# Performance work log

Measured on AMD Instinct MI355X. Metric: run time of the kernel, lower is better.

The kernel has to match this reference:

```python
import jax, jax.numpy as jnp
import numpy as np

TOP_K = 2

def setup_inputs() -> dict:
    key = jax.random.key(0)
    k1, k2 = jax.random.split(key)
    N, D, E = 16384, 2048, 64
    x = jax.random.normal(k1, (N, D), dtype=jnp.float32)
    W = jax.random.normal(k2, (D, E), dtype=jnp.float32) * (1.0 / np.sqrt(D))
    b = jnp.zeros((E,), dtype=jnp.float32)
    return {"x": x, "W": W, "b": b}

def reference(x, W, b):
    # gate linear: [N, D] @ [D, E] + [E]
    logits = jnp.einsum('nd,de->ne', x, W) + b
    gates = jax.nn.softmax(logits, axis=-1)
    topk_vals, topk_idx = jax.lax.top_k(gates, TOP_K)  # [N, k]
    N = gates.shape[0]
    rows = jnp.arange(N)[:, None]  # [N, 1] broadcast over k
    dispatch_mask = jnp.zeros_like(gates).at[rows, topk_idx].set(topk_vals)
    return dispatch_mask, topk_idx
```

## Files before the change

kernel.cpp:

```cpp
#include <hip/hip_runtime.h>
#include <math.h>

#define NROWS 16384
#define DDIM  2048
#define EEXP  64
#define RB    32
#define NST   8
#define CHSTRIDE 24576

typedef short        bf16x8 __attribute__((ext_vector_type(8)));
typedef float        f32x16 __attribute__((ext_vector_type(16)));
typedef float        f32x4  __attribute__((ext_vector_type(4)));
typedef unsigned int u32x4  __attribute__((ext_vector_type(4)));

union V4 { u32x4 u; bf16x8 s; };

static __device__ __forceinline__ void split3x2(float f0, float f1,
                                                unsigned int &p0, unsigned int &p1,
                                                unsigned int &p2) {
    unsigned int a0 = __float_as_uint(f0), b0 = __float_as_uint(f1);
    unsigned int ah = a0 & 0xffff0000u,   bh = b0 & 0xffff0000u;
    float fa1 = f0 - __uint_as_float(ah);
    float fb1 = f1 - __uint_as_float(bh);
    unsigned int a1 = __float_as_uint(fa1), b1 = __float_as_uint(fb1);
    unsigned int am = a1 & 0xffff0000u,     bm = b1 & 0xffff0000u;
    float fa2 = fa1 - __uint_as_float(am);
    float fb2 = fb1 - __uint_as_float(bm);
    p0 = (a0 >> 16) | bh;
    p1 = (a1 >> 16) | bm;
    p2 = (__float_as_uint(fa2) >> 16) | (__float_as_uint(fb2) & 0xffff0000u);
}

static __device__ __forceinline__ void cvt8(f32x4 u, f32x4 v, V4 &q0, V4 &q1, V4 &q2) {
    unsigned int a, b, c;
    split3x2(u[0], u[1], a, b, c); q0.u[0] = a; q1.u[0] = b; q2.u[0] = c;
    split3x2(u[2], u[3], a, b, c); q0.u[1] = a; q1.u[1] = b; q2.u[1] = c;
    split3x2(v[0], v[1], a, b, c); q0.u[2] = a; q1.u[2] = b; q2.u[2] = c;
    split3x2(v[2], v[3], a, b, c); q0.u[3] = a; q1.u[3] = b; q2.u[3] = c;
}

#define MM(ACC, A, B) ACC = __builtin_amdgcn_mfma_f32_32x32x16_bf16((A), (B), ACC, 0, 0, 0)

__global__ __launch_bounds__(256)
void wsplit_kernel(const float* __restrict__ W, unsigned char* __restrict__ ws) {
    const int t  = blockIdx.x * 256 + threadIdx.x;
    const int e  = t & 63;
    const int ko = t >> 6;
    const int k0 = ko * 8;
    f32x4 u, v;
#pragma unroll
    for (int j = 0; j < 4; ++j) u[j] = W[(size_t)(k0 + j) * EEXP + e];
#pragma unroll
    for (int j = 0; j < 4; ++j) v[j] = W[(size_t)(k0 + 4 + j) * EEXP + e];
    V4 q0, q1, q2;
    cvt8(u, v, q0, q1, q2);
    const int c  = k0 >> 6;
    const int kg = (k0 >> 4) & 3;
    const int h  = (k0 >> 3) & 1;
    const int et = e >> 5;
    const int ln = h * 32 + (e & 31);
    unsigned char* d = ws + (size_t)(((((c * 4 + kg) * 2 + et) * 64) + ln) * 48);
    *(u32x4*)(d +  0) = q0.u;
    *(u32x4*)(d + 16) = q1.u;
    *(u32x4*)(d + 32) = q2.u;
}

__global__ __launch_bounds__(512, 2)
void router_kernel(const float* __restrict__ x,
                   const unsigned char* __restrict__ wsplit,
                   const float* __restrict__ bias_v,
                   float* __restrict__ mask_out,
                   float* __restrict__ idx_out) {
    __shared__ __align__(16) float smem[16384];

    const int tid  = threadIdx.x;
    const int lane = tid & 63;
    const int w    = __builtin_amdgcn_readfirstlane(tid >> 6);
    const int kg   = w & 3;
    const int et   = w >> 2;
    const int l31  = lane & 31;
    const int h    = lane >> 5;

    const int bid  = blockIdx.x;
    const int bswz = (bid & 7) * ((int)gridDim.x >> 3) + (bid >> 3);
    const int row0 = bswz * RB;

    const int srow = 4 * w;

    const unsigned char* wp = wsplit + (size_t)(((kg * 2 + et) * 64 + lane) * 48);

    f32x16 accA, accB;
#pragma unroll
    for (int i = 0; i < 16; ++i) { accA[i] = 0.f; accB[i] = 0.f; }

    {
        f32x4 X0, X1, X2, X3;
        X0 = *(const f32x4*)(x + (size_t)(row0 + srow + 0) * DDIM + lane * 4);
        X1 = *(const f32x4*)(x + (size_t)(row0 + srow + 1) * DDIM + lane * 4);
        X2 = *(const f32x4*)(x + (size_t)(row0 + srow + 2) * DDIM + lane * 4);
        X3 = *(const f32x4*)(x + (size_t)(row0 + srow + 3) * DDIM + lane * 4);
#define XWR(I, V, B)                                                          \
        *(f32x4*)(smem + (B) * 8192 + (srow + I) * 256 +                      \
                  ((lane ^ ((srow + I) & 7)) << 2)) = V;
        XWR(0, X0, 0) XWR(1, X1, 0) XWR(2, X2, 0) XWR(3, X3, 0)
    }
    __syncthreads();

#pragma unroll 1
    for (int s = 0; s < NST; ++s) {
        const int  buf  = s & 1;
        const bool more = (s + 1) < NST;

        f32x4 X0, X1, X2, X3;
        if (more) {
            const float* xs = x + (size_t)(s + 1) * 256 + lane * 4;
            X0 = *(const f32x4*)(xs + (size_t)(row0 + srow + 0) * DDIM);
            X1 = *(const f32x4*)(xs + (size_t)(row0 + srow + 1) * DDIM);
            X2 = *(const f32x4*)(xs + (size_t)(row0 + srow + 2) * DDIM);
            X3 = *(const f32x4*)(xs + (size_t)(row0 + srow + 3) * DDIM);
        }

        const float* xb = smem + buf * 8192 + l31 * 256;
        const int xr = l31 & 7;
#pragma unroll
        for (int cc = 0; cc < 4; ++cc) {
            const int k0 = cc * 64 + kg * 16 + h * 8;
            const int bb = k0 >> 2;
            f32x4 lo = *(const f32x4*)(xb + (((bb    ) ^ xr) << 2));
            f32x4 hi = *(const f32x4*)(xb + (((bb + 1) ^ xr) << 2));
            const unsigned char* q = wp + (size_t)(s * 4 + cc) * CHSTRIDE;
            V4 b0, b1, b2;
            b0.u = *(const u32x4*)(q);
            b1.u = *(const u32x4*)(q + 16);
            b2.u = *(const u32x4*)(q + 32);
            V4 a0, a1, a2;
            cvt8(lo, hi, a0, a1, a2);
            MM(accA, a0.s, b0.s); MM(accB, a0.s, b1.s); MM(accA, a1.s, b0.s);
            MM(accB, a0.s, b2.s); MM(accA, a1.s, b1.s); MM(accB, a2.s, b0.s);
        }

        if (more) {
            const int nb = buf ^ 1;
            XWR(0, X0, nb) XWR(1, X1, nb) XWR(2, X2, nb) XWR(3, X3, nb)
        }
        __syncthreads();
    }

    float* ep = smem;
#pragma unroll
    for (int r = 0; r < 16; ++r) {
        const int rowl = (r & 3) + 8 * (r >> 2) + 4 * h;
        ep[kg * 2048 + rowl * 64 + et * 32 + l31] = accA[r] + accB[r];
    }
    __syncthreads();

    const float bias = bias_v[lane];
#pragma unroll
    for (int rr = 0; rr < 4; ++rr) {
        const int rl  = w * 4 + rr;
        const int row = row0 + rl;
        float logit = bias + ep[rl * 64 + lane]
                           + ep[2048 + rl * 64 + lane]
                           + ep[4096 + rl * 64 + lane]
                           + ep[6144 + rl * 64 + lane];

        float m = logit;
#pragma unroll
        for (int off = 32; off >= 1; off >>= 1) m = fmaxf(m, __shfl_xor(m, off));
        float ex = __expf(logit - m);
        float s = ex;
#pragma unroll
        for (int off = 32; off >= 1; off >>= 1) s += __shfl_xor(s, off);
        float gate = ex / s;

        float v1 = logit; int i1 = lane;
#pragma unroll
        for (int off = 32; off >= 1; off >>= 1) {
            float ov = __shfl_xor(v1, off);
            int   oi = __shfl_xor(i1, off);
            if (ov > v1 || (ov == v1 && oi < i1)) { v1 = ov; i1 = oi; }
        }
        float v2 = (lane == i1) ? -INFINITY : logit; int i2 = lane;
#pragma unroll
        for (int off = 32; off >= 1; off >>= 1) {
            float ov = __shfl_xor(v2, off);
            int   oi = __shfl_xor(i2, off);
            if (ov > v2 || (ov == v2 && oi < i2)) { v2 = ov; i2 = oi; }
        }

        float outv = (lane == i1 || lane == i2) ? gate : 0.0f;
        mask_out[(size_t)row * EEXP + lane] = outv;
        if (lane == 0) {
            idx_out[row * 2 + 0] = (float)i1;
            idx_out[row * 2 + 1] = (float)i2;
        }
    }
}

extern "C" void kernel_launch(void* const* d_in, const int* in_sizes, int n_in,
                              void* d_out, int out_size, void* d_ws, size_t ws_size,
                              hipStream_t stream) {
    const float* x = (const float*)d_in[0];
    const float* W = (const float*)d_in[1];
    const float* b = (const float*)d_in[2];
    float* mask_out = (float*)d_out;
    float* idx_out  = mask_out + (size_t)NROWS * EEXP;
    unsigned char* ws = (unsigned char*)d_ws;

    wsplit_kernel<<<dim3(64), dim3(256), 0, stream>>>(W, ws);
    router_kernel<<<dim3(NROWS / RB), dim3(512), 0, stream>>>(x, ws, b, mask_out, idx_out);
}
```

Measured before the change: 212.3 us.

## Double rows per block to reuse W fragments and stagger K-stage order

Each block now handles 64 rows instead of 32. Every wave keeps two sets of accumulators, so each W split fragment loaded from global memory feeds twice as many MFMAs. Blocks also start the K loop at different stages (s0 = block index mod 8) to spread W reads across memory channels. In exchange, LDS doubles to 128KB per block, accumulator and register pressure grow, and the grid is halved to 256 blocks, which may cut occupancy and parallelism on the 256-CU device.

```diff
diff --git a/kernel.cpp b/kernel.cpp
--- a/kernel.cpp
+++ b/kernel.cpp
@@ -4,7 +4,7 @@
 #define NROWS 16384
 #define DDIM  2048
 #define EEXP  64
-#define RB    32
+#define RB    64
 #define NST   8
 #define CHSTRIDE 24576
 
@@ -71,7 +71,7 @@
                    const float* __restrict__ bias_v,
                    float* __restrict__ mask_out,
                    float* __restrict__ idx_out) {
-    __shared__ __align__(16) float smem[16384];
+    __shared__ __align__(16) float smem[32768];
 
     const int tid  = threadIdx.x;
     const int lane = tid & 63;
@@ -84,64 +84,84 @@
     const int bid  = blockIdx.x;
     const int bswz = (bid & 7) * ((int)gridDim.x >> 3) + (bid >> 3);
     const int row0 = bswz * RB;
-
-    const int srow = 4 * w;
+    const int s0   = bswz & 7;
+
+    const int srow = 8 * w;
 
     const unsigned char* wp = wsplit + (size_t)(((kg * 2 + et) * 64 + lane) * 48);
 
-    f32x16 accA, accB;
-#pragma unroll
-    for (int i = 0; i < 16; ++i) { accA[i] = 0.f; accB[i] = 0.f; }
+    f32x16 accA, accB, accC, accD;
+#pragma unroll
+    for (int i = 0; i < 16; ++i) { accA[i] = 0.f; accB[i] = 0.f; accC[i] = 0.f; accD[i] = 0.f; }
+
+#define XWR(I, V, B, SR_ROW_BASE)                                             \
+    *(f32x4*)(smem + (B) * 16384 + (SR_ROW_BASE + I) * 256 +                  \
+              ((lane ^ ((SR_ROW_BASE + I) & 7)) << 2)) = V;
 
     {
-        f32x4 X0, X1, X2, X3;
-        X0 = *(const f32x4*)(x + (size_t)(row0 + srow + 0) * DDIM + lane * 4);
-        X1 = *(const f32x4*)(x + (size_t)(row0 + srow + 1) * DDIM + lane * 4);
-        X2 = *(const f32x4*)(x + (size_t)(row0 + srow + 2) * DDIM + lane * 4);
-        X3 = *(const f32x4*)(x + (size_t)(row0 + srow + 3) * DDIM + lane * 4);
-#define XWR(I, V, B)                                                          \
-        *(f32x4*)(smem + (B) * 8192 + (srow + I) * 256 +                      \
-                  ((lane ^ ((srow + I) & 7)) << 2)) = V;
-        XWR(0, X0, 0) XWR(1, X1, 0) XWR(2, X2, 0) XWR(3, X3, 0)
+        const float* xs = x + (size_t)s0 * 256 + lane * 4;
+        f32x4 X0 = *(const f32x4*)(xs + (size_t)(row0 + srow + 0) * DDIM);
+        f32x4 X1 = *(const f32x4*)(xs + (size_t)(row0 + srow + 1) * DDIM);
+        f32x4 X2 = *(const f32x4*)(xs + (size_t)(row0 + srow + 2) * DDIM);
+        f32x4 X3 = *(const f32x4*)(xs + (size_t)(row0 + srow + 3) * DDIM);
+        f32x4 X4 = *(const f32x4*)(xs + (size_t)(row0 + srow + 4) * DDIM);
+        f32x4 X5 = *(const f32x4*)(xs + (size_t)(row0 + srow + 5) * DDIM);
+        f32x4 X6 = *(const f32x4*)(xs + (size_t)(row0 + srow + 6) * DDIM);
+        f32x4 X7 = *(const f32x4*)(xs + (size_t)(row0 + srow + 7) * DDIM);
+        XWR(0, X0, 0, srow) XWR(1, X1, 0, srow) XWR(2, X2, 0, srow) XWR(3, X3, 0, srow)
+        XWR(4, X4, 0, srow) XWR(5, X5, 0, srow) XWR(6, X6, 0, srow) XWR(7, X7, 0, srow)
     }
     __syncthreads();
 
 #pragma unroll 1
     for (int s = 0; s < NST; ++s) {
         const int  buf  = s & 1;
+        const int  sr   = (s0 + s) & 7;
         const bool more = (s + 1) < NST;
 
-        f32x4 X0, X1, X2, X3;
+        f32x4 X0, X1, X2, X3, X4, X5, X6, X7;
         if (more) {
-            const float* xs = x + (size_t)(s + 1) * 256 + lane * 4;
+            const int srn = (s0 + s + 1) & 7;
+            const float* xs = x + (size_t)srn * 256 + lane * 4;
             X0 = *(const f32x4*)(xs + (size_t)(row0 + srow + 0) * DDIM);
             X1 = *(const f32x4*)(xs + (size_t)(row0 + srow + 1) * DDIM);
             X2 = *(const f32x4*)(xs + (size_t)(row0 + srow + 2) * DDIM);
             X3 = *(const f32x4*)(xs + (size_t)(row0 + srow + 3) * DDIM);
-        }
-
-        const float* xb = smem + buf * 8192 + l31 * 256;
+            X4 = *(const f32x4*)(xs + (size_t)(row0 + srow + 4) * DDIM);
+            X5 = *(const f32x4*)(xs + (size_t)(row0 + srow + 5) * DDIM);
+            X6 = *(const f32x4*)(xs + (size_t)(row0 + srow + 6) * DDIM);
+            X7 = *(const f32x4*)(xs + (size_t)(row0 + srow + 7) * DDIM);
+        }
+
+        const float* xb0 = smem + buf * 16384 + l31 * 256;
+        const float* xb1 = xb0 + 32 * 256;
         const int xr = l31 & 7;
 #pragma unroll
         for (int cc = 0; cc < 4; ++cc) {
             const int k0 = cc * 64 + kg * 16 + h * 8;
             const int bb = k0 >> 2;
-            f32x4 lo = *(const f32x4*)(xb + (((bb    ) ^ xr) << 2));
-            f32x4 hi = *(const f32x4*)(xb + (((bb + 1) ^ xr) << 2));
-            const unsigned char* q = wp + (size_t)(s * 4 + cc) * CHSTRIDE;
+            f32x4 lo0 = *(const f32x4*)(xb0 + (((bb    ) ^ xr) << 2));
+            f32x4 hi0 = *(const f32x4*)(xb0 + (((bb + 1) ^ xr) << 2));
+            f32x4 lo1 = *(const f32x4*)(xb1 + (((bb    ) ^ xr) << 2));
+            f32x4 hi1 = *(const f32x4*)(xb1 + (((bb + 1) ^ xr) << 2));
+            const unsigned char* q = wp + (size_t)(sr * 4 + cc) * CHSTRIDE;
             V4 b0, b1, b2;
             b0.u = *(const u32x4*)(q);
             b1.u = *(const u32x4*)(q + 16);
             b2.u = *(const u32x4*)(q + 32);
             V4 a0, a1, a2;
-            cvt8(lo, hi, a0, a1, a2);
+            cvt8(lo0, hi0, a0, a1, a2);
             MM(accA, a0.s, b0.s); MM(accB, a0.s, b1.s); MM(accA, a1.s, b0.s);
             MM(accB, a0.s, b2.s); MM(accA, a1.s, b1.s); MM(accB, a2.s, b0.s);
+            cvt8(lo1, hi1, a0, a1, a2);
+            MM(accC, a0.s, b0.s); MM(accD, a0.s, b1.s); MM(accC, a1.s, b0.s);
+            MM(accD, a0.s, b2.s); MM(accC, a1.s, b1.s); MM(accD, a2.s, b0.s);
         }
 
         if (more) {
             const int nb = buf ^ 1;
-            XWR(0, X0, nb) XWR(1, X1, nb) XWR(2, X2, nb) XWR(3, X3, nb)
+            XWR(0, X0, nb, srow) XWR(1, X1, nb, srow) XWR(2, X2, nb, srow) XWR(3, X3, nb, srow)
+            XWR(4, X4, nb, srow) XWR(5, X5, nb, srow) XWR(6, X6, nb, srow) XWR(7, X7, nb, srow)
         }
         __syncthreads();
     }
@@ -150,19 +170,20 @@
 #pragma unroll
     for (int r = 0; r < 16; ++r) {
         const int rowl = (r & 3) + 8 * (r >> 2) + 4 * h;
-        ep[kg * 2048 + rowl * 64 + et * 32 + l31] = accA[r] + accB[r];
+        ep[kg * 4096 + rowl * 64 + et * 32 + l31]        = accA[r] + accB[r];
+        ep[kg * 4096 + (rowl + 32) * 64 + et * 32 + l31] = accC[r] + accD[r];
     }
     __syncthreads();
 
     const float bias = bias_v[lane];
 #pragma unroll
-    for (int rr = 0; rr < 4; ++rr) {
-        const int rl  = w * 4 + rr;
+    for (int rr = 0; rr < 8; ++rr) {
+        const int rl  = w * 8 + rr;
         const int row = row0 + rl;
         float logit = bias + ep[rl * 64 + lane]
-                           + ep[2048 + rl * 64 + lane]
-                           + ep[4096 + rl * 64 + lane]
-                           + ep[6144 + rl * 64 + lane];
+                           + ep[4096  + rl * 64 + lane]
+                           + ep[8192  + rl * 64 + lane]
+                           + ep[12288 + rl * 64 + lane];
 
         float m = logit;
 #pragma unroll
```

Result: no change. 216.0 us (+1.8%).

## Stream x tiles via global_load_lds and make split-W loads lane-contiguous

Applied to the files above, without the earlier changes.

Replaces the register-staged x prefetch (global load into VGPRs, then LDS store after the MFMA loop) with direct global-to-LDS loads. The XOR swizzle is moved onto the global source address so the LDS layout stays the same. The precomputed bf16-split W workspace is re-laid out into three planes of 1024 bytes, so each lane's 16-byte loads of b0/b1/b2 are contiguous across the wavefront rather than strided by 48 bytes. The aim is to cut VGPR pressure and LDS write instructions and to improve load coalescing. The risk is that global_load_lds ordering depends on the barrier placement, and the compiler's wait-count handling for it may add stalls.

```diff
diff --git a/kernel.cpp b/kernel.cpp
--- a/kernel.cpp
+++ b/kernel.cpp
@@ -54,15 +54,15 @@
     for (int j = 0; j < 4; ++j) v[j] = W[(size_t)(k0 + 4 + j) * EEXP + e];
     V4 q0, q1, q2;
     cvt8(u, v, q0, q1, q2);
-    const int c  = k0 >> 6;
-    const int kg = (k0 >> 4) & 3;
-    const int h  = (k0 >> 3) & 1;
+    const int c  = ko >> 3;
+    const int kg = (ko >> 1) & 3;
+    const int h  = ko & 1;
     const int et = e >> 5;
     const int ln = h * 32 + (e & 31);
-    unsigned char* d = ws + (size_t)(((((c * 4 + kg) * 2 + et) * 64) + ln) * 48);
-    *(u32x4*)(d +  0) = q0.u;
-    *(u32x4*)(d + 16) = q1.u;
-    *(u32x4*)(d + 32) = q2.u;
+    unsigned char* d = ws + (size_t)((c * 8 + kg * 2 + et) * 3) * 1024 + ln * 16;
+    *(u32x4*)(d +    0) = q0.u;
+    *(u32x4*)(d + 1024) = q1.u;
+    *(u32x4*)(d + 2048) = q2.u;
 }
 
 __global__ __launch_bounds__(512, 2)
@@ -87,37 +87,32 @@
 
     const int srow = 4 * w;
 
-    const unsigned char* wp = wsplit + (size_t)(((kg * 2 + et) * 64 + lane) * 48);
+#define GLL(I, BAND, BUF)                                                     \
+    __builtin_amdgcn_global_load_lds(                                         \
+        (const __attribute__((address_space(1))) void*)                       \
+            (x + (size_t)(row0 + srow + (I)) * DDIM + (BAND)                  \
+               + ((lane ^ ((srow + (I)) & 7)) << 2)),                         \
+        (__attribute__((address_space(3))) void*)                             \
+            (smem + (BUF) * 8192 + (srow + (I)) * 256),                       \
+        16, 0, 0);
+
+    const unsigned char* wq = wsplit + (size_t)((kg * 2 + et) * 3) * 1024 + lane * 16;
 
     f32x16 accA, accB;
 #pragma unroll
     for (int i = 0; i < 16; ++i) { accA[i] = 0.f; accB[i] = 0.f; }
 
-    {
-        f32x4 X0, X1, X2, X3;
-        X0 = *(const f32x4*)(x + (size_t)(row0 + srow + 0) * DDIM + lane * 4);
-        X1 = *(const f32x4*)(x + (size_t)(row0 + srow + 1) * DDIM + lane * 4);
-        X2 = *(const f32x4*)(x + (size_t)(row0 + srow + 2) * DDIM + lane * 4);
-        X3 = *(const f32x4*)(x + (size_t)(row0 + srow + 3) * DDIM + lane * 4);
-#define XWR(I, V, B)                                                          \
-        *(f32x4*)(smem + (B) * 8192 + (srow + I) * 256 +                      \
-                  ((lane ^ ((srow + I) & 7)) << 2)) = V;
-        XWR(0, X0, 0) XWR(1, X1, 0) XWR(2, X2, 0) XWR(3, X3, 0)
-    }
+    GLL(0, 0, 0) GLL(1, 0, 0) GLL(2, 0, 0) GLL(3, 0, 0)
     __syncthreads();
 
 #pragma unroll 1
     for (int s = 0; s < NST; ++s) {
-        const int  buf  = s & 1;
-        const bool more = (s + 1) < NST;
-
-        f32x4 X0, X1, X2, X3;
-        if (more) {
-            const float* xs = x + (size_t)(s + 1) * 256 + lane * 4;
-            X0 = *(const f32x4*)(xs + (size_t)(row0 + srow + 0) * DDIM);
-            X1 = *(const f32x4*)(xs + (size_t)(row0 + srow + 1) * DDIM);
-            X2 = *(const f32x4*)(xs + (size_t)(row0 + srow + 2) * DDIM);
-            X3 = *(const f32x4*)(xs + (size_t)(row0 + srow + 3) * DDIM);
+        const int buf = s & 1;
+
+        if (s + 1 < NST) {
+            const int band = (s + 1) * 256;
+            const int nb = buf ^ 1;
+            GLL(0, band, nb) GLL(1, band, nb) GLL(2, band, nb) GLL(3, band, nb)
         }
 
         const float* xb = smem + buf * 8192 + l31 * 256;
@@ -128,21 +123,17 @@
             const int bb = k0 >> 2;
             f32x4 lo = *(const f32x4*)(xb + (((bb    ) ^ xr) << 2));
             f32x4 hi = *(const f32x4*)(xb + (((bb + 1) ^ xr) << 2));
-            const unsigned char* q = wp + (size_t)(s * 4 + cc) * CHSTRIDE;
+            const unsigned char* q = wq + (size_t)(s * 4 + cc) * CHSTRIDE;
             V4 b0, b1, b2;
             b0.u = *(const u32x4*)(q);
-            b1.u = *(const u32x4*)(q + 16);
-            b2.u = *(const u32x4*)(q + 32);
+            b1.u = *(const u32x4*)(q + 1024);
+            b2.u = *(const u32x4*)(q + 2048);
             V4 a0, a1, a2;
             cvt8(lo, hi, a0, a1, a2);
             MM(accA, a0.s, b0.s); MM(accB, a0.s, b1.s); MM(accA, a1.s, b0.s);
             MM(accB, a0.s, b2.s); MM(accA, a1.s, b1.s); MM(accB, a2.s, b0.s);
         }
 
-        if (more) {
-            const int nb = buf ^ 1;
-            XWR(0, X0, nb) XWR(1, X1, nb) XWR(2, X2, nb) XWR(3, X3, nb)
-        }
         __syncthreads();
     }
 
```

New measurement: 207.8 us. -2.1%, faster.
